# Kernel optimization log

Hardware: AMD Instinct MI355X
Metric: run time of the kernel (lower is better)

Reference implementation:

```python
import jax, jax.numpy as jnp
import numpy as np

N_NODES = 20000
N_EDGES = 640000
D = 128


def setup_inputs() -> dict:
    key = jax.random.key(0)
    ks = jax.random.split(key, 8)
    scale = 1.0 / np.sqrt(D)
    x = jax.random.normal(ks[0], (N_NODES, D), dtype=jnp.float32)
    edge_index = jax.random.randint(ks[1], (2, N_EDGES), 0, N_NODES, dtype=jnp.int64)
    W1_rel = jax.random.normal(ks[2], (D, D), dtype=jnp.float32) * scale
    b1_rel = jnp.zeros((D,), dtype=jnp.float32)
    W1_root = jax.random.normal(ks[3], (D, D), dtype=jnp.float32) * scale
    W2_rel = jax.random.normal(ks[4], (D, D), dtype=jnp.float32) * scale
    b2_rel = jnp.zeros((D,), dtype=jnp.float32)
    W2_root = jax.random.normal(ks[5], (D, D), dtype=jnp.float32) * scale
    return {"x": x, "edge_index": edge_index,
            "W1_rel": W1_rel, "b1_rel": b1_rel, "W1_root": W1_root,
            "W2_rel": W2_rel, "b2_rel": b2_rel, "W2_root": W2_root}


def _graph_conv(x, src, dst, W_rel, b_rel, W_root):
    # sum-aggregate neighbor features: gather from src, scatter-add to dst
    agg = jax.ops.segment_sum(x[src], dst, num_segments=N_NODES)  # [N, D]
    # PyG GraphConv: lin_rel(agg) (with bias) + lin_root(x) (no bias)
    return agg @ W_rel + b_rel + x @ W_root


def reference(x, edge_index, W1_rel, b1_rel, W1_root, W2_rel, b2_rel, W2_root):
    src, dst = edge_index[0], edge_index[1]  # messages flow src (j) -> dst (i)
    h = jax.nn.relu(_graph_conv(x, src, dst, W1_rel, b1_rel, W1_root))
    out = _graph_conv(h, src, dst, W2_rel, b2_rel, W2_root)  # final ReLU stripped
    return out
```

## Files before the change

### kernel.cpp

```cpp
#include <hip/hip_runtime.h>

#define N_NODES 20000
#define N_EDGES 640000
#define D 128
#define CAP 128
#define NBINS 625
#define PA_BLOCKS 256
#define EPB 2500
#define SLABCAP 24
#define SRC_SPLIT 10000

typedef __attribute__((ext_vector_type(8))) short bf16x8;
typedef __attribute__((ext_vector_type(4))) float f32x4;

__device__ __forceinline__ short f2bf(float f) {
    union { float f; unsigned u; } un; un.f = f;
    unsigned r = un.u + 0x7fff + ((un.u >> 16) & 1);
    return (short)(r >> 16);
}
__device__ __forceinline__ float bflo(unsigned u) { return __uint_as_float(u << 16); }
__device__ __forceinline__ float bfhi(unsigned u) { return __uint_as_float(u & 0xffff0000u); }

__global__ __launch_bounds__(256) void prep_kernel(
    const float* __restrict__ x,
    const int* __restrict__ src, const int* __restrict__ dst,
    const float* __restrict__ W1_rel, const float* __restrict__ W1_root,
    const float* __restrict__ W2_rel, const float* __restrict__ W2_root,
    unsigned* __restrict__ binned, int* __restrict__ cnts,
    short* __restrict__ xb, short* __restrict__ wpk1, short* __restrict__ wpk2)
{
    const int b = blockIdx.x;
    const int tid = threadIdx.x;
    if (b < PA_BLOCKS) {
        __shared__ int sOff[NBINS];
        for (int i = tid; i < NBINS; i += 256) sOff[i] = 0;
        __syncthreads();
        const int e0 = b * EPB;
        for (int idx = tid; idx < EPB; idx += 256) {
            int d = dst[e0 + idx];
            int s = src[e0 + idx];
            int bin = d >> 5;
            int off = atomicAdd(&sOff[bin], 1);
            if (off < SLABCAP)
                binned[((size_t)b * NBINS + bin) * SLABCAP + off] =
                    ((unsigned)(d & 31) << 16) | (unsigned)s;
        }
        __syncthreads();
        for (int i = tid; i < NBINS; i += 256) {
            int c = sOff[i];
            cnts[b * NBINS + i] = (c > SLABCAP) ? SLABCAP : c;
        }
    } else if (b < PA_BLOCKS + 2500) {
        int i = (b - PA_BLOCKS) * 256 + tid;
        float4 v = ((const float4*)x)[i];
        ushort4 o;
        o.x = (unsigned short)f2bf(v.x);
        o.y = (unsigned short)f2bf(v.y);
        o.z = (unsigned short)f2bf(v.z);
        o.w = (unsigned short)f2bf(v.w);
        ((ushort4*)xb)[i] = o;
    } else {
        int pb  = b - (PA_BLOCKS + 2500);
        int job = pb >> 4;
        int idx = (pb & 15) * 256 + tid;
        const float* Wrel  = job ? W2_rel  : W1_rel;
        const float* Wroot = job ? W2_root : W1_root;
        short* Wpk = job ? wpk2 : wpk1;
        int lane = idx & 63;
        int ct   = (idx >> 6) & 7;
        int t    = idx >> 9;
        const float* W = (t < 4) ? Wrel : Wroot;
        int k0  = (t & 3) * 32 + (lane >> 4) * 8;
        int col = ct * 16 + (lane & 15);
        bf16x8 pk;
#pragma unroll
        for (int j = 0; j < 8; j++)
            pk[j] = f2bf(W[(size_t)(k0 + j) * D + col]);
        ((bf16x8*)Wpk)[idx] = pk;
    }
}

__device__ __forceinline__ void gather16(
    float (&accf)[8], const short* __restrict__ xin,
    const unsigned short* __restrict__ bkt, int l16, int start, int count)
{
    const int end  = start + count;
    const int fend = start + (count & ~7);
    int k = start;
    for (; k < fend; k += 8) {
        uint4 u[8];
#pragma unroll
        for (int q = 0; q < 8; q++) {
            unsigned sidx = bkt[k + q];
            u[q] = *(const uint4*)(xin + (size_t)sidx * D + l16 * 8);
        }
#pragma unroll
        for (int q = 0; q < 8; q++) {
            accf[0] += bflo(u[q].x); accf[1] += bfhi(u[q].x);
            accf[2] += bflo(u[q].y); accf[3] += bfhi(u[q].y);
            accf[4] += bflo(u[q].z); accf[5] += bfhi(u[q].z);
            accf[6] += bflo(u[q].w); accf[7] += bfhi(u[q].w);
        }
    }
    if (k < end) {
        uint4 u[8];
#pragma unroll
        for (int q = 0; q < 8; q++) {
            int j  = k + q;
            int jc = (j < end) ? j : (end - 1);
            unsigned sidx = bkt[jc];
            u[q] = *(const uint4*)(xin + (size_t)sidx * D + l16 * 8);
        }
#pragma unroll
        for (int q = 0; q < 8; q++) {
            float m = (k + q < end) ? 1.f : 0.f;
            accf[0] += m * bflo(u[q].x); accf[1] += m * bfhi(u[q].x);
            accf[2] += m * bflo(u[q].y); accf[3] += m * bfhi(u[q].y);
            accf[4] += m * bflo(u[q].z); accf[5] += m * bfhi(u[q].z);
            accf[6] += m * bflo(u[q].w); accf[7] += m * bfhi(u[q].w);
        }
    }
}

template <bool RELU, bool OUT_BF16>
__global__ __launch_bounds__(512, 4) void layer_kernel(
    const short* __restrict__ xin,
    const unsigned* __restrict__ binned,
    const int* __restrict__ cnts,
    const short* __restrict__ Wpk,
    const float* __restrict__ brel,
    void* __restrict__ outp)
{
    __shared__ unsigned short sBkt[32][CAP + 2];
    __shared__ short sAgg[32][136];
    __shared__ int lo[32], hi[32];

    const int tid  = threadIdx.x;
    const int g    = blockIdx.x;
    const int row0 = g * 32;

    if (tid < 32) { lo[tid] = 0; hi[tid] = 0; }
    __syncthreads();
    if (tid < PA_BLOCKS) {
        int c = cnts[tid * NBINS + g];
        const unsigned* rec = binned + ((size_t)tid * NBINS + g) * SLABCAP;
        for (int i = 0; i < c; i++) {
            unsigned u = rec[i];
            int nl = (int)(u >> 16);
            unsigned s = u & 0xffffu;
            if ((int)s < SRC_SPLIT) {
                int slot = atomicAdd(&lo[nl], 1);
                if (slot < CAP) sBkt[nl][slot] = (unsigned short)s;
            } else {
                int slot = CAP - 1 - atomicAdd(&hi[nl], 1);
                if (slot >= 0) sBkt[nl][slot] = (unsigned short)s;
            }
        }
    }
    __syncthreads();

    {
        const int node = tid >> 4;
        const int l16  = tid & 15;
        int nlo = lo[node]; if (nlo > CAP) nlo = CAP;
        int nhi = hi[node]; if (nhi > CAP - nlo) nhi = CAP - nlo;

        float accf[8];
#pragma unroll
        for (int j = 0; j < 8; j++) accf[j] = 0.f;

        gather16(accf, xin, sBkt[node], l16, 0, nlo);
        __syncthreads();
        gather16(accf, xin, sBkt[node], l16, CAP - nhi, nhi);

        bf16x8 pk;
#pragma unroll
        for (int j = 0; j < 8; j++) pk[j] = f2bf(accf[j]);
        *(bf16x8*)&sAgg[node][l16 * 8] = pk;
    }
    __syncthreads();

    const int wave = tid >> 6;
    const int lane = tid & 63;
    const int quad = lane >> 4;
    const int l16  = lane & 15;

    f32x4 acc0 = (f32x4){0.f, 0.f, 0.f, 0.f};
    f32x4 acc1 = (f32x4){0.f, 0.f, 0.f, 0.f};
    const short* ax0 = xin + (size_t)(row0 + l16) * D + quad * 8;
    const short* ax1 = xin + (size_t)(row0 + 16 + l16) * D + quad * 8;
    const bf16x8* wb = (const bf16x8*)Wpk + lane;

#pragma unroll
    for (int t = 0; t < 8; t++) {
        bf16x8 bfr = wb[(t * 8 + wave) * 64];
        bf16x8 a0, a1;
        if (t < 4) {
            a0 = *(const bf16x8*)&sAgg[l16][(t & 3) * 32 + quad * 8];
            a1 = *(const bf16x8*)&sAgg[16 + l16][(t & 3) * 32 + quad * 8];
        } else {
            a0 = *(const bf16x8*)(ax0 + (t & 3) * 32);
            a1 = *(const bf16x8*)(ax1 + (t & 3) * 32);
        }
        acc0 = __builtin_amdgcn_mfma_f32_16x16x32_bf16(a0, bfr, acc0, 0, 0, 0);
        acc1 = __builtin_amdgcn_mfma_f32_16x16x32_bf16(a1, bfr, acc1, 0, 0, 0);
    }

    const int col  = wave * 16 + l16;
    const float bias = brel[col];
#pragma unroll
    for (int r = 0; r < 4; r++) {
        float v0 = acc0[r] + bias;
        float v1 = acc1[r] + bias;
        if (RELU) { v0 = fmaxf(v0, 0.f); v1 = fmaxf(v1, 0.f); }
        int o0 = row0 + quad * 4 + r;
        int o1 = o0 + 16;
        if (OUT_BF16) {
            ((short*)outp)[(size_t)o0 * D + col] = f2bf(v0);
            ((short*)outp)[(size_t)o1 * D + col] = f2bf(v1);
        } else {
            ((float*)outp)[(size_t)o0 * D + col] = v0;
            ((float*)outp)[(size_t)o1 * D + col] = v1;
        }
    }
}

extern "C" void kernel_launch(void* const* d_in, const int* in_sizes, int n_in,
                              void* d_out, int out_size, void* d_ws, size_t ws_size,
                              hipStream_t stream) {
    const float* x       = (const float*)d_in[0];
    const int*   ei      = (const int*)  d_in[1];
    const float* W1_rel  = (const float*)d_in[2];
    const float* b1_rel  = (const float*)d_in[3];
    const float* W1_root = (const float*)d_in[4];
    const float* W2_rel  = (const float*)d_in[5];
    const float* b2_rel  = (const float*)d_in[6];
    const float* W2_root = (const float*)d_in[7];
    float* out = (float*)d_out;

    char* p = (char*)d_ws;
    short* xb   = (short*)p;  p += (size_t)N_NODES * D * 2;
    short* hb   = (short*)p;  p += (size_t)N_NODES * D * 2;
    short* wpk1 = (short*)p;  p += 65536;
    short* wpk2 = (short*)p;  p += 65536;
    unsigned* binned = (unsigned*)p;
    p += (size_t)PA_BLOCKS * NBINS * SLABCAP * 4;
    int* cnts = (int*)p;

    const int* src = ei;
    const int* dst = ei + N_EDGES;

    prep_kernel<<<PA_BLOCKS + 2500 + 32, 256, 0, stream>>>(
        x, src, dst, W1_rel, W1_root, W2_rel, W2_root,
        binned, cnts, xb, wpk1, wpk2);

    layer_kernel<true, true><<<NBINS, 512, 0, stream>>>(
        xb, binned, cnts, wpk1, b1_rel, (void*)hb);

    layer_kernel<false, false><<<NBINS, 512, 0, stream>>>(
        hb, binned, cnts, wpk2, b2_rel, (void*)out);
}
```

Before: 150.5 us.

## Split gather into two column-half kernels and cache per-node bucket lists globally

Each layer's neighbor aggregation is split into two passes. The first kernel gathers feature columns 0-63 to a global buffer, and the second gathers columns 64-127 and then runs the MFMA matmul. Halving the columns per pass shrinks the working set of the random gathers so more of it stays in cache. The sorted per-node source buckets are built once in layer 1 and saved to global memory, so later kernels reload them instead of re-binning. In exchange there are more kernel launches and extra global traffic for the agg0 and bucket buffers.

```diff
diff --git a/kernel.cpp b/kernel.cpp
--- a/kernel.cpp
+++ b/kernel.cpp
@@ -80,82 +80,143 @@
     }
 }
 
-__device__ __forceinline__ void gather16(
-    float (&accf)[8], const short* __restrict__ xin,
+__device__ __forceinline__ void gather_u2(
+    float (&accf)[4], const short* __restrict__ colbase,
     const unsigned short* __restrict__ bkt, int l16, int start, int count)
 {
     const int end  = start + count;
     const int fend = start + (count & ~7);
     int k = start;
     for (; k < fend; k += 8) {
-        uint4 u[8];
+        uint2 u[8];
 #pragma unroll
         for (int q = 0; q < 8; q++) {
             unsigned sidx = bkt[k + q];
-            u[q] = *(const uint4*)(xin + (size_t)sidx * D + l16 * 8);
+            u[q] = *(const uint2*)(colbase + (size_t)sidx * D + l16 * 4);
         }
 #pragma unroll
         for (int q = 0; q < 8; q++) {
             accf[0] += bflo(u[q].x); accf[1] += bfhi(u[q].x);
             accf[2] += bflo(u[q].y); accf[3] += bfhi(u[q].y);
-            accf[4] += bflo(u[q].z); accf[5] += bfhi(u[q].z);
-            accf[6] += bflo(u[q].w); accf[7] += bfhi(u[q].w);
         }
     }
     if (k < end) {
-        uint4 u[8];
+        uint2 u[8];
 #pragma unroll
         for (int q = 0; q < 8; q++) {
             int j  = k + q;
             int jc = (j < end) ? j : (end - 1);
             unsigned sidx = bkt[jc];
-            u[q] = *(const uint4*)(xin + (size_t)sidx * D + l16 * 8);
+            u[q] = *(const uint2*)(colbase + (size_t)sidx * D + l16 * 4);
         }
 #pragma unroll
         for (int q = 0; q < 8; q++) {
             float m = (k + q < end) ? 1.f : 0.f;
             accf[0] += m * bflo(u[q].x); accf[1] += m * bfhi(u[q].x);
             accf[2] += m * bflo(u[q].y); accf[3] += m * bfhi(u[q].y);
-            accf[4] += m * bflo(u[q].z); accf[5] += m * bfhi(u[q].z);
-            accf[6] += m * bflo(u[q].w); accf[7] += m * bfhi(u[q].w);
-        }
-    }
-}
-
-template <bool RELU, bool OUT_BF16>
-__global__ __launch_bounds__(512, 4) void layer_kernel(
+        }
+    }
+}
+
+template <bool BUILD>
+__global__ __launch_bounds__(512, 4) void gatherA_kernel(
     const short* __restrict__ xin,
-    const unsigned* __restrict__ binned,
-    const int* __restrict__ cnts,
-    const short* __restrict__ Wpk,
-    const float* __restrict__ brel,
-    void* __restrict__ outp)
+    const unsigned* __restrict__ binned, const int* __restrict__ cnts,
+    unsigned short* __restrict__ gBkt, int* __restrict__ gCnt,
+    short* __restrict__ agg0)
 {
-    __shared__ unsigned short sBkt[32][CAP + 2];
-    __shared__ short sAgg[32][136];
+    __shared__ unsigned short sBkt[32][CAP + 8];
     __shared__ int lo[32], hi[32];
 
     const int tid  = threadIdx.x;
     const int g    = blockIdx.x;
     const int row0 = g * 32;
 
-    if (tid < 32) { lo[tid] = 0; hi[tid] = 0; }
-    __syncthreads();
-    if (tid < PA_BLOCKS) {
-        int c = cnts[tid * NBINS + g];
-        const unsigned* rec = binned + ((size_t)tid * NBINS + g) * SLABCAP;
-        for (int i = 0; i < c; i++) {
-            unsigned u = rec[i];
-            int nl = (int)(u >> 16);
-            unsigned s = u & 0xffffu;
-            if ((int)s < SRC_SPLIT) {
-                int slot = atomicAdd(&lo[nl], 1);
-                if (slot < CAP) sBkt[nl][slot] = (unsigned short)s;
-            } else {
-                int slot = CAP - 1 - atomicAdd(&hi[nl], 1);
-                if (slot >= 0) sBkt[nl][slot] = (unsigned short)s;
+    if (BUILD) {
+        if (tid < 32) { lo[tid] = 0; hi[tid] = 0; }
+        __syncthreads();
+        if (tid < PA_BLOCKS) {
+            int c = cnts[tid * NBINS + g];
+            const unsigned* rec = binned + ((size_t)tid * NBINS + g) * SLABCAP;
+            for (int i = 0; i < c; i++) {
+                unsigned u = rec[i];
+                int nl = (int)(u >> 16);
+                unsigned s = u & 0xffffu;
+                if ((int)s < SRC_SPLIT) {
+                    int slot = atomicAdd(&lo[nl], 1);
+                    if (slot < CAP) sBkt[nl][slot] = (unsigned short)s;
+                } else {
+                    int slot = CAP - 1 - atomicAdd(&hi[nl], 1);
+                    if (slot >= 0) sBkt[nl][slot] = (unsigned short)s;
+                }
             }
         }
+        __syncthreads();
+        {
+            int r = tid >> 4, c = (tid & 15) * 8;
+            *(uint4*)(gBkt + (size_t)(row0 + r) * CAP + c) =
+                *(const uint4*)&sBkt[r][c];
+        }
+        if (tid < 32) {
+            int nlo = lo[tid]; if (nlo > CAP) nlo = CAP;
+            int nhi = hi[tid]; if (nhi > CAP - nlo) nhi = CAP - nlo;
+            gCnt[row0 + tid] = nlo | (nhi << 16);
+        }
+    } else {
+        {
+            int r = tid >> 4, c = (tid & 15) * 8;
+            *(uint4*)&sBkt[r][c] =
+                *(const uint4*)(gBkt + (size_t)(row0 + r) * CAP + c);
+        }
+        if (tid < 32) {
+            int pc = gCnt[row0 + tid];
+            lo[tid] = pc & 0xffff; hi[tid] = pc >> 16;
+        }
+        __syncthreads();
+    }
+    if (BUILD) __syncthreads();
+
+    const int node = tid >> 4;
+    const int l16  = tid & 15;
+    int nlo = lo[node]; if (nlo > CAP) nlo = CAP;
+    int nhi = hi[node]; if (nhi > CAP - nlo) nhi = CAP - nlo;
+
+    float accf[4] = {0.f, 0.f, 0.f, 0.f};
+    gather_u2(accf, xin, sBkt[node], l16, 0, nlo);
+    gather_u2(accf, xin, sBkt[node], l16, CAP - nhi, nhi);
+
+    ushort4 o;
+    o.x = (unsigned short)f2bf(accf[0]);
+    o.y = (unsigned short)f2bf(accf[1]);
+    o.z = (unsigned short)f2bf(accf[2]);
+    o.w = (unsigned short)f2bf(accf[3]);
+    *(ushort4*)(agg0 + (size_t)(row0 + node) * 64 + l16 * 4) = o;
+}
+
+template <bool RELU, bool OUT_BF16>
+__global__ __launch_bounds__(512, 4) void layerB_kernel(
+    const short* __restrict__ xin,
+    const unsigned short* __restrict__ gBkt, const int* __restrict__ gCnt,
+    const short* __restrict__ agg0,
+    const short* __restrict__ Wpk, const float* __restrict__ brel,
+    void* __restrict__ outp)
+{
+    __shared__ unsigned short sBkt[32][CAP + 8];
+    __shared__ short sAgg1[32][72];
+    __shared__ int lo[32], hi[32];
+
+    const int tid  = threadIdx.x;
+    const int g    = blockIdx.x;
+    const int row0 = g * 32;
+
+    {
+        int r = tid >> 4, c = (tid & 15) * 8;
+        *(uint4*)&sBkt[r][c] =
+            *(const uint4*)(gBkt + (size_t)(row0 + r) * CAP + c);
+    }
+    if (tid < 32) {
+        int pc = gCnt[row0 + tid];
+        lo[tid] = pc & 0xffff; hi[tid] = pc >> 16;
     }
     __syncthreads();
 
@@ -165,18 +226,16 @@
         int nlo = lo[node]; if (nlo > CAP) nlo = CAP;
         int nhi = hi[node]; if (nhi > CAP - nlo) nhi = CAP - nlo;
 
-        float accf[8];
-#pragma unroll
-        for (int j = 0; j < 8; j++) accf[j] = 0.f;
-
-        gather16(accf, xin, sBkt[node], l16, 0, nlo);
-        __syncthreads();
-        gather16(accf, xin, sBkt[node], l16, CAP - nhi, nhi);
-
-        bf16x8 pk;
-#pragma unroll
-        for (int j = 0; j < 8; j++) pk[j] = f2bf(accf[j]);
-        *(bf16x8*)&sAgg[node][l16 * 8] = pk;
+        float accf[4] = {0.f, 0.f, 0.f, 0.f};
+        gather_u2(accf, xin + 64, sBkt[node], l16, 0, nlo);
+        gather_u2(accf, xin + 64, sBkt[node], l16, CAP - nhi, nhi);
+
+        ushort4 o;
+        o.x = (unsigned short)f2bf(accf[0]);
+        o.y = (unsigned short)f2bf(accf[1]);
+        o.z = (unsigned short)f2bf(accf[2]);
+        o.w = (unsigned short)f2bf(accf[3]);
+        *(ushort4*)&sAgg1[node][l16 * 4] = o;
     }
     __syncthreads();
 
@@ -189,15 +248,20 @@
     f32x4 acc1 = (f32x4){0.f, 0.f, 0.f, 0.f};
     const short* ax0 = xin + (size_t)(row0 + l16) * D + quad * 8;
     const short* ax1 = xin + (size_t)(row0 + 16 + l16) * D + quad * 8;
+    const short* ag0 = agg0 + (size_t)(row0 + l16) * 64 + quad * 8;
+    const short* ag1 = agg0 + (size_t)(row0 + 16 + l16) * 64 + quad * 8;
     const bf16x8* wb = (const bf16x8*)Wpk + lane;
 
 #pragma unroll
     for (int t = 0; t < 8; t++) {
         bf16x8 bfr = wb[(t * 8 + wave) * 64];
         bf16x8 a0, a1;
-        if (t < 4) {
-            a0 = *(const bf16x8*)&sAgg[l16][(t & 3) * 32 + quad * 8];
-            a1 = *(const bf16x8*)&sAgg[16 + l16][(t & 3) * 32 + quad * 8];
+        if (t < 2) {
+            a0 = *(const bf16x8*)(ag0 + (t & 1) * 32);
+            a1 = *(const bf16x8*)(ag1 + (t & 1) * 32);
+        } else if (t < 4) {
+            a0 = *(const bf16x8*)&sAgg1[l16][(t & 1) * 32 + quad * 8];
+            a1 = *(const bf16x8*)&sAgg1[16 + l16][(t & 1) * 32 + quad * 8];
         } else {
             a0 = *(const bf16x8*)(ax0 + (t & 3) * 32);
             a1 = *(const bf16x8*)(ax1 + (t & 3) * 32);
@@ -243,6 +307,10 @@
     short* hb   = (short*)p;  p += (size_t)N_NODES * D * 2;
     short* wpk1 = (short*)p;  p += 65536;
     short* wpk2 = (short*)p;  p += 65536;
+    short* agg0 = (short*)p;  p += (size_t)N_NODES * 64 * 2;
+    unsigned short* gBkt = (unsigned short*)p;
+    p += (size_t)N_NODES * CAP * 2;
+    int* gCnt = (int*)p;      p += (size_t)N_NODES * 4;
     unsigned* binned = (unsigned*)p;
     p += (size_t)PA_BLOCKS * NBINS * SLABCAP * 4;
     int* cnts = (int*)p;
@@ -254,9 +322,13 @@
         x, src, dst, W1_rel, W1_root, W2_rel, W2_root,
         binned, cnts, xb, wpk1, wpk2);
 
-    layer_kernel<true, true><<<NBINS, 512, 0, stream>>>(
-        xb, binned, cnts, wpk1, b1_rel, (void*)hb);
-
-    layer_kernel<false, false><<<NBINS, 512, 0, stream>>>(
-        hb, binned, cnts, wpk2, b2_rel, (void*)out);
-}
+    gatherA_kernel<true><<<NBINS, 512, 0, stream>>>(
+        xb, binned, cnts, gBkt, gCnt, agg0);
+    layerB_kernel<true, true><<<NBINS, 512, 0, stream>>>(
+        xb, gBkt, gCnt, agg0, wpk1, b1_rel, (void*)hb);
+
+    gatherA_kernel<false><<<NBINS, 512, 0, stream>>>(
+        hb, binned, cnts, gBkt, gCnt, agg0);
+    layerB_kernel<false, false><<<NBINS, 512, 0, stream>>>(
+        hb, gBkt, gCnt, agg0, wpk2, b2_rel, (void*)out);
+}
```

New measurement: 162.2 us. +7.7%, slower.
